# Optimization experiments

Measured on AMD Instinct MI355X. Metric: run time of the kernel, lower is better.

Reference implementation:

```python
import jax, jax.numpy as jnp
import numpy as np

QMIN, QMAX = -128.0, 127.0          # int-8 symmetric range
CONST_N = 15.0                      # shift-exp range constant
OUT_BIT = 8                         # const_output_bit
INT32_MAX = 2.0 ** 31 - 1.0


def setup_inputs() -> dict:
    key = jax.random.key(0)
    kx, ks = jax.random.split(key)
    x = jax.random.normal(kx, (4, 2048, 4096), dtype=jnp.float32)
    # per-channel quantizer scale ~ abs-max / 127 statistics
    scaler = jnp.max(jnp.abs(x), axis=(0, 1)) / 127.0 + 1e-6  # [D]
    return {"x": x, "scaler": scaler}


def _int_exp_shift(x_int, sf):
    # x_int ~ integer-valued float tensor; sf per-channel scaling factor [D]
    x_int = x_int + jnp.floor(x_int / 2.0) - jnp.floor(x_int / 16.0)  # *1.4375 ~ /ln2
    x0 = jnp.floor(-1.0 / sf)                     # [D], negative
    x_int = jnp.maximum(x_int, CONST_N * x0)
    q = jnp.floor(x_int / x0)
    r = x_int - x0 * q
    e = r / 2.0 - x0
    return jnp.maximum(jnp.floor(e * jnp.exp2(CONST_N - q)), 0.0)


def reference(x, scaler):
    # quantize input per-channel (int8 grid, kept in float)
    pre_x_int = jnp.clip(jnp.round(x / scaler), QMIN, QMAX)
    sf_sig = scaler * 1.702

    x_int_max = jnp.max(pre_x_int, axis=-1, keepdims=True)   # [B,S,1]
    x_int = pre_x_int - x_int_max

    exp_int = _int_exp_shift(x_int, sf_sig)                  # [B,S,D]
    exp_int_max = _int_exp_shift(-x_int_max, sf_sig)         # [B,S,D] (bcast)
    exp_sum = jnp.minimum(exp_int + exp_int_max, INT32_MAX)

    factor = jnp.floor(INT32_MAX / exp_sum)
    sigmoid_int = jnp.floor(exp_int * factor / 2.0 ** (31 - OUT_BIT + 1))

    sigmoid_scale = 1.0 / 2.0 ** (OUT_BIT - 1)    # 1/128
    y = pre_x_int * sigmoid_int * (scaler * sigmoid_scale)
    return y
```

## Files before the change

kernel.cpp:

```cpp
#include <hip/hip_runtime.h>


#define D 4096
#define BLK 512
#define CPT 8
#define RPB 8
#define NW (BLK / 64)
#define NSLOT 12
#define TENT (NSLOT * 256)
#define EPS 1e-4f
#define F2_31 2147483648.0f

typedef float f32x4 __attribute__((ext_vector_type(4)));

__device__ __forceinline__ float exp_fast(float xi, float nx0, float rx0) {
    const float q = floorf(fmaf(xi, rx0, EPS));
    const float r = fmaf(nx0, q, xi);
    const float e = fmaf(r, 0.5f, nx0);
    return floorf(ldexpf(e, 15 - (int)q));
}

__device__ __forceinline__ float exp_slow(float xi, float x0) {
    xi = fmaxf(xi, 15.0f * x0);
    const float q = floorf(xi / x0);
    const float r = fmaf(-x0, q, xi);
    const float e = fmaf(r, 0.5f, -x0);
    return fmaxf(floorf(e * ldexpf(1.0f, 15 - (int)q)), 0.0f);
}

__global__ __launch_bounds__(BLK) void quantgelu_kernel(
    const float* __restrict__ x, const float* __restrict__ scaler,
    float* __restrict__ out, int nrows)
{
    const int tid  = threadIdx.x;
    const int wid  = tid >> 6;
    const int lane = tid & 63;
    const int row0 = blockIdx.x * RPB;

    __shared__ __align__(16) float smax2[2][NW];
    __shared__ float eit[TENT];
    __shared__ float sig2[2][TENT];

    const int c0 = tid * 4;
    const int c1 = BLK * 4 + tid * 4;

    float4 xv[2];
    if (row0 < nrows) {
        const long long b0 = (long long)row0 * D;
        xv[0] = *reinterpret_cast<const float4*>(x + b0 + c0);
        xv[1] = *reinterpret_cast<const float4*>(x + b0 + c1);
    }

    float s_[CPT], rs_[CPT];
    int   bo_[CPT];
    float x0mn, x0mx;
    {
        float x0t[CPT];
        #pragma unroll
        for (int k = 0; k < 2; ++k) {
            const float4 sv = *reinterpret_cast<const float4*>(scaler + (k ? c1 : c0));
            const float ss[4] = {sv.x, sv.y, sv.z, sv.w};
            #pragma unroll
            for (int j = 0; j < 4; ++j) {
                const int i = k * 4 + j;
                const float s = ss[j];
                s_[i]  = s;
                rs_[i] = 1.0f / s;
                x0t[i] = floorf(-1.0f / (s * 1.702f));
            }
        }
        x0mn = x0t[0]; x0mx = x0t[0];
        #pragma unroll
        for (int i = 1; i < CPT; ++i) {
            x0mn = fminf(x0mn, x0t[i]);
            x0mx = fmaxf(x0mx, x0t[i]);
        }
        #pragma unroll
        for (int off = 1; off < 64; off <<= 1) {
            x0mn = fminf(x0mn, __shfl_xor(x0mn, off));
            x0mx = fmaxf(x0mx, __shfl_xor(x0mx, off));
        }
        if (lane == 0) { smax2[0][wid] = x0mn; smax2[1][wid] = x0mx; }
        __syncthreads();
        #pragma unroll
        for (int w = 0; w < NW; ++w) {
            x0mn = fminf(x0mn, smax2[0][w]);
            x0mx = fmaxf(x0mx, smax2[1][w]);
        }
        __syncthreads();

        #pragma unroll
        for (int i = 0; i < CPT; ++i)
            bo_[i] = ((int)(x0t[i] - x0mn)) << 8;
    }

    const int  nslots = (int)(x0mx - x0mn) + 1;
    const bool ok = (x0mn >= -64.0f) && (nslots <= NSLOT);
    const int  nent = nslots << 8;

    const float x0l  = x0mn + (float)lane;
    const float nx0l = -x0l;
    const float rx0l = 1.0f / x0l;
    const float c15l = 15.0f * x0l;

    if (ok) {
        for (int e = tid; e < nent; e += BLK) {
            const int   slot = e >> 8;
            const float x0v  = x0mn + (float)slot;
            float xi = -(float)(e & 255);
            xi = xi + floorf(xi * 0.5f) - floorf(xi * 0.0625f);
            xi = fmaxf(xi, 15.0f * x0v);
            eit[e] = exp_fast(xi, -x0v, __shfl(rx0l, slot));
        }
    }

    float pre_c[CPT], pre_n[CPT];
    float vmax = -INFINITY;
    if (row0 < nrows) {
        #pragma unroll
        for (int k = 0; k < 2; ++k) {
            const float* xa = reinterpret_cast<const float*>(&xv[k]);
            #pragma unroll
            for (int j = 0; j < 4; ++j) {
                const int i = k * 4 + j;
                const float q0 = xa[j] * rs_[i];
                const float rr = fmaf(-s_[i], q0, xa[j]);
                const float p  = __builtin_amdgcn_fmed3f(
                                   rintf(fmaf(rr, rs_[i], q0)), -128.0f, 127.0f);
                pre_c[i] = p;
                vmax = fmaxf(vmax, p);
            }
        }
        #pragma unroll
        for (int off = 1; off < 64; off <<= 1)
            vmax = fmaxf(vmax, __shfl_xor(vmax, off));
        if (lane == 0) smax2[0][wid] = vmax;
        if (row0 + 1 < nrows) {
            const long long b1 = (long long)(row0 + 1) * D;
            xv[0] = *reinterpret_cast<const float4*>(x + b1 + c0);
            xv[1] = *reinterpret_cast<const float4*>(x + b1 + c1);
        }
    }
    __syncthreads();
    {
        const float4 a0 = *reinterpret_cast<const float4*>(&smax2[0][0]);
        const float4 a1 = *reinterpret_cast<const float4*>(&smax2[0][4]);
        vmax = fmaxf(fmaxf(fmaxf(a0.x, a0.y), fmaxf(a0.z, a0.w)),
                     fmaxf(fmaxf(a1.x, a1.y), fmaxf(a1.z, a1.w)));
    }

    for (int r = 0; r < RPB; ++r) {
        const int row = row0 + r;
        if (row >= nrows) break;
        const bool hasnext = (r + 1 < RPB) && (row + 1 < nrows);
        const int  cur = r & 1, nxt = cur ^ 1;

        const float xm  = -vmax;
        const float xmt = xm + floorf(xm * 0.5f) - floorf(xm * 0.0625f);

        if (ok) {
            const float em_l = exp_fast(fmaxf(xmt, c15l), nx0l, rx0l);
            for (int e = tid; e < nent; e += BLK) {
                const int   slot = e >> 8;
                const float ei   = eit[e];
                const float em   = __shfl(em_l, slot);
                const float f    = floorf(F2_31 / fminf(ei + em, F2_31));
                sig2[cur][e] = floorf((ei * f) * 0x1p-24f) * 0.0078125f;
            }
        }

        if (hasnext) {
            float vnext = -INFINITY;
            #pragma unroll
            for (int k = 0; k < 2; ++k) {
                const float* xa = reinterpret_cast<const float*>(&xv[k]);
                #pragma unroll
                for (int j = 0; j < 4; ++j) {
                    const int i = k * 4 + j;
                    const float q0 = xa[j] * rs_[i];
                    const float rr = fmaf(-s_[i], q0, xa[j]);
                    const float p  = __builtin_amdgcn_fmed3f(
                                       rintf(fmaf(rr, rs_[i], q0)), -128.0f, 127.0f);
                    pre_n[i] = p;
                    vnext = fmaxf(vnext, p);
                }
            }
            #pragma unroll
            for (int off = 1; off < 64; off <<= 1)
                vnext = fmaxf(vnext, __shfl_xor(vnext, off));
            if (lane == 0) smax2[nxt][wid] = vnext;
            if (r + 2 < RPB && row + 2 < nrows) {
                const long long b2 = (long long)(row + 2) * D;
                xv[0] = *reinterpret_cast<const float4*>(x + b2 + c0);
                xv[1] = *reinterpret_cast<const float4*>(x + b2 + c1);
            }
        }

        __syncthreads();

        const long long rb = (long long)row * D;
        if (ok) {
            #pragma unroll
            for (int k = 0; k < 2; ++k) {
                f32x4 ov;
                #pragma unroll
                for (int j = 0; j < 4; ++j) {
                    const int i = k * 4 + j;
                    const int d = (int)(vmax - pre_c[i]);
                    ov[j] = (pre_c[i] * sig2[cur][bo_[i] + d]) * s_[i];
                }
                __builtin_nontemporal_store(
                    ov, reinterpret_cast<f32x4*>(out + rb + (k ? c1 : c0)));
            }
        } else {
            #pragma unroll
            for (int k = 0; k < 2; ++k) {
                f32x4 ov;
                #pragma unroll
                for (int j = 0; j < 4; ++j) {
                    const int i = k * 4 + j;
                    const float x0 = floorf(-1.0f / (s_[i] * 1.702f));
                    float xi = pre_c[i] - vmax;
                    xi = xi + floorf(xi * 0.5f) - floorf(xi * 0.0625f);
                    const float ei = exp_slow(xi, x0);
                    const float em = exp_slow(xmt, x0);
                    const float factor = floorf(F2_31 / fminf(ei + em, F2_31));
                    ov[j] = (pre_c[i] * floorf((ei * factor) * 0x1p-24f))
                            * (s_[i] * 0.0078125f);
                }
                __builtin_nontemporal_store(
                    ov, reinterpret_cast<f32x4*>(out + rb + (k ? c1 : c0)));
            }
        }

        if (hasnext) {
            const float4 a0 = *reinterpret_cast<const float4*>(&smax2[nxt][0]);
            const float4 a1 = *reinterpret_cast<const float4*>(&smax2[nxt][4]);
            vmax = fmaxf(fmaxf(fmaxf(a0.x, a0.y), fmaxf(a0.z, a0.w)),
                         fmaxf(fmaxf(a1.x, a1.y), fmaxf(a1.z, a1.w)));
            #pragma unroll
            for (int i = 0; i < CPT; ++i) pre_c[i] = pre_n[i];
        }
    }
}

extern "C" void kernel_launch(void* const* d_in, const int* in_sizes, int n_in,
                              void* d_out, int out_size, void* d_ws, size_t ws_size,
                              hipStream_t stream) {
    const float* x      = (const float*)d_in[0];
    const float* scaler = (const float*)d_in[1];
    float* out          = (float*)d_out;

    const int nrows = in_sizes[0] / D;
    const int grid  = (nrows + RPB - 1) / RPB;
    quantgelu_kernel<<<grid, BLK, 0, stream>>>(x, scaler, out, nrows);
}
```

Measured before the change: 49.37 us.

## Halve block size, pack quantized values into bytes, drop double-buffered sigmoid table

Block size drops to 256 threads, each handling 16 columns, and each block now covers 4 rows instead of 8. The quantized int8 values and per-channel slot indices are packed four to a 32-bit register, and scaler values are reloaded from memory instead of kept in registers. The double-buffered shared sigmoid table is replaced by a single table, and the slot count is cut to 9. The aim is lower register and LDS pressure for higher occupancy. In exchange the software pipelining across rows is lost, since each row's max reduction is now serialized, and there is extra scaler reloading and byte unpacking.

New measurement: 102.9 us. 2.09x slower.

```diff
diff --git a/kernel.cpp b/kernel.cpp
--- a/kernel.cpp
+++ b/kernel.cpp
@@ -2,11 +2,11 @@
 
 
 #define D 4096
-#define BLK 512
-#define CPT 8
-#define RPB 8
+#define BLK 256
+#define CPT 16
+#define RPB 4
 #define NW (BLK / 64)
-#define NSLOT 12
+#define NSLOT 9
 #define TENT (NSLOT * 256)
 #define EPS 1e-4f
 #define F2_31 2147483648.0f
@@ -37,66 +37,70 @@
     const int lane = tid & 63;
     const int row0 = blockIdx.x * RPB;
 
+    __shared__ float eit[TENT];
+    __shared__ float sigt[TENT];
     __shared__ __align__(16) float smax2[2][NW];
-    __shared__ float eit[TENT];
-    __shared__ float sig2[2][TENT];
-
-    const int c0 = tid * 4;
-    const int c1 = BLK * 4 + tid * 4;
-
-    float4 xv[2];
+
+
+    float4 xv[4];
     if (row0 < nrows) {
         const long long b0 = (long long)row0 * D;
-        xv[0] = *reinterpret_cast<const float4*>(x + b0 + c0);
-        xv[1] = *reinterpret_cast<const float4*>(x + b0 + c1);
-    }
-
-    float s_[CPT], rs_[CPT];
-    int   bo_[CPT];
+        #pragma unroll
+        for (int k = 0; k < 4; ++k)
+            xv[k] = *reinterpret_cast<const float4*>(x + b0 + k * 1024 + tid * 4);
+    }
+
+    float rs_[CPT];
     float x0mn, x0mx;
     {
-        float x0t[CPT];
-        #pragma unroll
-        for (int k = 0; k < 2; ++k) {
-            const float4 sv = *reinterpret_cast<const float4*>(scaler + (k ? c1 : c0));
+        float mn = 1.0f, mx = -1e30f;
+        #pragma unroll
+        for (int k = 0; k < 4; ++k) {
+            const float4 sv = *reinterpret_cast<const float4*>(scaler + k * 1024 + tid * 4);
             const float ss[4] = {sv.x, sv.y, sv.z, sv.w};
             #pragma unroll
             for (int j = 0; j < 4; ++j) {
-                const int i = k * 4 + j;
                 const float s = ss[j];
-                s_[i]  = s;
-                rs_[i] = 1.0f / s;
-                x0t[i] = floorf(-1.0f / (s * 1.702f));
-            }
-        }
-        x0mn = x0t[0]; x0mx = x0t[0];
-        #pragma unroll
-        for (int i = 1; i < CPT; ++i) {
-            x0mn = fminf(x0mn, x0t[i]);
-            x0mx = fmaxf(x0mx, x0t[i]);
+                rs_[k * 4 + j] = 1.0f / s;
+                const float x0 = floorf(-1.0f / (s * 1.702f));
+                mn = fminf(mn, x0);
+                mx = fmaxf(mx, x0);
+            }
         }
         #pragma unroll
         for (int off = 1; off < 64; off <<= 1) {
-            x0mn = fminf(x0mn, __shfl_xor(x0mn, off));
-            x0mx = fmaxf(x0mx, __shfl_xor(x0mx, off));
-        }
-        if (lane == 0) { smax2[0][wid] = x0mn; smax2[1][wid] = x0mx; }
-        __syncthreads();
+            mn = fminf(mn, __shfl_xor(mn, off));
+            mx = fmaxf(mx, __shfl_xor(mx, off));
+        }
+        if (lane == 0) { smax2[0][wid] = mn; smax2[1][wid] = mx; }
+        __syncthreads();
+        x0mn = mn; x0mx = mx;
         #pragma unroll
         for (int w = 0; w < NW; ++w) {
             x0mn = fminf(x0mn, smax2[0][w]);
             x0mx = fmaxf(x0mx, smax2[1][w]);
         }
         __syncthreads();
-
-        #pragma unroll
-        for (int i = 0; i < CPT; ++i)
-            bo_[i] = ((int)(x0t[i] - x0mn)) << 8;
     }
 
     const int  nslots = (int)(x0mx - x0mn) + 1;
     const bool ok = (x0mn >= -64.0f) && (nslots <= NSLOT);
     const int  nent = nslots << 8;
+
+    unsigned slotpk[4];
+    #pragma unroll
+    for (int k = 0; k < 4; ++k) {
+        const float4 sv = *reinterpret_cast<const float4*>(scaler + k * 1024 + tid * 4);
+        const float ss[4] = {sv.x, sv.y, sv.z, sv.w};
+        unsigned b = 0u;
+        #pragma unroll
+        for (int j = 0; j < 4; ++j) {
+            const float x0 = floorf(-1.0f / (ss[j] * 1.702f));
+            const float sl = fminf(fmaxf(x0 - x0mn, 0.0f), 255.0f);
+            b |= ((unsigned)(int)sl & 0xffu) << (8 * j);
+        }
+        slotpk[k] = b;
+    }
 
     const float x0l  = x0mn + (float)lane;
     const float nx0l = -x0l;
@@ -114,49 +118,51 @@
         }
     }
 
-    float pre_c[CPT], pre_n[CPT];
-    float vmax = -INFINITY;
-    if (row0 < nrows) {
-        #pragma unroll
-        for (int k = 0; k < 2; ++k) {
+    for (int r = 0; r < RPB; ++r) {
+        const int row = row0 + r;
+        if (row >= nrows) break;
+        const long long rb = (long long)row * D;
+
+        float vmax = -INFINITY;
+        unsigned pk[4];
+        #pragma unroll
+        for (int k = 0; k < 4; ++k) {
+            const float4 sv = *reinterpret_cast<const float4*>(scaler + k * 1024 + tid * 4);
+            const float ss[4] = {sv.x, sv.y, sv.z, sv.w};
             const float* xa = reinterpret_cast<const float*>(&xv[k]);
+            unsigned b = 0u;
             #pragma unroll
             for (int j = 0; j < 4; ++j) {
                 const int i = k * 4 + j;
                 const float q0 = xa[j] * rs_[i];
-                const float rr = fmaf(-s_[i], q0, xa[j]);
+                const float rr = fmaf(-ss[j], q0, xa[j]);
                 const float p  = __builtin_amdgcn_fmed3f(
-                                   rintf(fmaf(rr, rs_[i], q0)), -128.0f, 127.0f);
-                pre_c[i] = p;
+                                    rintf(fmaf(rr, rs_[i], q0)), -128.0f, 127.0f);
                 vmax = fmaxf(vmax, p);
-            }
-        }
+                b |= ((unsigned)(int)p & 0xffu) << (8 * j);
+            }
+            pk[k] = b;
+        }
+
+        if (r + 1 < RPB && row + 1 < nrows) {
+            #pragma unroll
+            for (int k = 0; k < 4; ++k)
+                xv[k] = *reinterpret_cast<const float4*>(x + rb + D + k * 1024 + tid * 4);
+        }
+
         #pragma unroll
         for (int off = 1; off < 64; off <<= 1)
             vmax = fmaxf(vmax, __shfl_xor(vmax, off));
         if (lane == 0) smax2[0][wid] = vmax;
-        if (row0 + 1 < nrows) {
-            const long long b1 = (long long)(row0 + 1) * D;
-            xv[0] = *reinterpret_cast<const float4*>(x + b1 + c0);
-            xv[1] = *reinterpret_cast<const float4*>(x + b1 + c1);
-        }
-    }
-    __syncthreads();
-    {
-        const float4 a0 = *reinterpret_cast<const float4*>(&smax2[0][0]);
-        const float4 a1 = *reinterpret_cast<const float4*>(&smax2[0][4]);
-        vmax = fmaxf(fmaxf(fmaxf(a0.x, a0.y), fmaxf(a0.z, a0.w)),
-                     fmaxf(fmaxf(a1.x, a1.y), fmaxf(a1.z, a1.w)));
-    }
-
-    for (int r = 0; r < RPB; ++r) {
-        const int row = row0 + r;
-        if (row >= nrows) break;
-        const bool hasnext = (r + 1 < RPB) && (row + 1 < nrows);
-        const int  cur = r & 1, nxt = cur ^ 1;
+        __syncthreads();
+        {
+            const float4 a = *reinterpret_cast<const float4*>(&smax2[0][0]);
+            vmax = fmaxf(fmaxf(a.x, a.y), fmaxf(a.z, a.w));
+        }
 
         const float xm  = -vmax;
         const float xmt = xm + floorf(xm * 0.5f) - floorf(xm * 0.0625f);
+        const int   vmi = (int)vmax;
 
         if (ok) {
             const float em_l = exp_fast(fmaxf(xmt, c15l), nx0l, rx0l);
@@ -165,81 +171,47 @@
                 const float ei   = eit[e];
                 const float em   = __shfl(em_l, slot);
                 const float f    = floorf(F2_31 / fminf(ei + em, F2_31));
-                sig2[cur][e] = floorf((ei * f) * 0x1p-24f) * 0.0078125f;
-            }
-        }
-
-        if (hasnext) {
-            float vnext = -INFINITY;
-            #pragma unroll
-            for (int k = 0; k < 2; ++k) {
-                const float* xa = reinterpret_cast<const float*>(&xv[k]);
-                #pragma unroll
-                for (int j = 0; j < 4; ++j) {
-                    const int i = k * 4 + j;
-                    const float q0 = xa[j] * rs_[i];
-                    const float rr = fmaf(-s_[i], q0, xa[j]);
-                    const float p  = __builtin_amdgcn_fmed3f(
-                                       rintf(fmaf(rr, rs_[i], q0)), -128.0f, 127.0f);
-                    pre_n[i] = p;
-                    vnext = fmaxf(vnext, p);
-                }
-            }
-            #pragma unroll
-            for (int off = 1; off < 64; off <<= 1)
-                vnext = fmaxf(vnext, __shfl_xor(vnext, off));
-            if (lane == 0) smax2[nxt][wid] = vnext;
-            if (r + 2 < RPB && row + 2 < nrows) {
-                const long long b2 = (long long)(row + 2) * D;
-                xv[0] = *reinterpret_cast<const float4*>(x + b2 + c0);
-                xv[1] = *reinterpret_cast<const float4*>(x + b2 + c1);
-            }
-        }
-
-        __syncthreads();
-
-        const long long rb = (long long)row * D;
+                sigt[e] = floorf((ei * f) * 0x1p-24f) * 0.0078125f;
+            }
+        }
+        __syncthreads();
+
         if (ok) {
             #pragma unroll
-            for (int k = 0; k < 2; ++k) {
+            for (int k = 0; k < 4; ++k) {
+                const float4 sv = *reinterpret_cast<const float4*>(scaler + k * 1024 + tid * 4);
+                const float ss[4] = {sv.x, sv.y, sv.z, sv.w};
                 f32x4 ov;
                 #pragma unroll
                 for (int j = 0; j < 4; ++j) {
-                    const int i = k * 4 + j;
-                    const int d = (int)(vmax - pre_c[i]);
-                    ov[j] = (pre_c[i] * sig2[cur][bo_[i] + d]) * s_[i];
+                    const int pi = (int)(signed char)((pk[k] >> (8 * j)) & 0xffu);
+                    const int sl = (int)((slotpk[k] >> (8 * j)) & 0xffu);
+                    ov[j] = ((float)pi * sigt[(sl << 8) + (vmi - pi)]) * ss[j];
                 }
                 __builtin_nontemporal_store(
-                    ov, reinterpret_cast<f32x4*>(out + rb + (k ? c1 : c0)));
+                    ov, reinterpret_cast<f32x4*>(out + rb + k * 1024 + tid * 4));
             }
         } else {
             #pragma unroll
-            for (int k = 0; k < 2; ++k) {
+            for (int k = 0; k < 4; ++k) {
+                const float4 sv = *reinterpret_cast<const float4*>(scaler + k * 1024 + tid * 4);
+                const float ss[4] = {sv.x, sv.y, sv.z, sv.w};
                 f32x4 ov;
                 #pragma unroll
                 for (int j = 0; j < 4; ++j) {
-                    const int i = k * 4 + j;
-                    const float x0 = floorf(-1.0f / (s_[i] * 1.702f));
-                    float xi = pre_c[i] - vmax;
+                    const float x0 = floorf(-1.0f / (ss[j] * 1.702f));
+                    const float pf = (float)(int)(signed char)((pk[k] >> (8 * j)) & 0xffu);
+                    float xi = pf - vmax;
                     xi = xi + floorf(xi * 0.5f) - floorf(xi * 0.0625f);
                     const float ei = exp_slow(xi, x0);
                     const float em = exp_slow(xmt, x0);
                     const float factor = floorf(F2_31 / fminf(ei + em, F2_31));
-                    ov[j] = (pre_c[i] * floorf((ei * factor) * 0x1p-24f))
-                            * (s_[i] * 0.0078125f);
+                    ov[j] = (pf * floorf((ei * factor) * 0x1p-24f))
+                            * (ss[j] * 0.0078125f);
                 }
                 __builtin_nontemporal_store(
-                    ov, reinterpret_cast<f32x4*>(out + rb + (k ? c1 : c0)));
-            }
-        }
-
-        if (hasnext) {
-            const float4 a0 = *reinterpret_cast<const float4*>(&smax2[nxt][0]);
-            const float4 a1 = *reinterpret_cast<const float4*>(&smax2[nxt][4]);
-            vmax = fmaxf(fmaxf(fmaxf(a0.x, a0.y), fmaxf(a0.z, a0.w)),
-                         fmaxf(fmaxf(a1.x, a1.y), fmaxf(a1.z, a1.w)));
-            #pragma unroll
-            for (int i = 0; i < CPT; ++i) pre_c[i] = pre_n[i];
+                    ov, reinterpret_cast<f32x4*>(out + rb + k * 1024 + tid * 4));
+            }
         }
     }
 }
```
